# Performance work log

Measured on AMD Instinct MI355X. Metric: run time of the kernel, lower is better.

## Reference

```python
import jax, jax.numpy as jnp
import numpy as np

HEADS = 8
DIM_HEAD = 64
SCALE = DIM_HEAD ** -0.5
THRESH = 0.01


def setup_inputs() -> dict:
    key = jax.random.key(0)
    ks = jax.random.split(key, 5)
    b, n, dim = 4, 2048, 512
    inner = HEADS * DIM_HEAD  # 512
    x = jax.random.normal(ks[0], (b, n, dim), dtype=jnp.float32)
    Wqkv = jax.random.normal(ks[1], (dim, 3 * inner), dtype=jnp.float32) * (dim ** -0.5)
    bqkv = jax.random.normal(ks[2], (3 * inner,), dtype=jnp.float32) * 0.02
    Wout = jax.random.normal(ks[3], (inner, dim), dtype=jnp.float32) * (inner ** -0.5)
    bout = jax.random.normal(ks[4], (dim,), dtype=jnp.float32) * 0.02
    return {"x": x, "Wqkv": Wqkv, "bqkv": bqkv, "Wout": Wout, "bout": bout}


def reference(x, Wqkv, bqkv, Wout, bout):
    b, n, dim = x.shape
    qkv = x @ Wqkv + bqkv  # [b, n, 3*inner]
    q, k, v = jnp.split(qkv, 3, axis=-1)
    # b n (h d) -> b h n d
    split_heads = lambda t: t.reshape(b, n, HEADS, DIM_HEAD).transpose(0, 2, 1, 3)
    q, k, v = split_heads(q), split_heads(k), split_heads(v)
    dots = jnp.einsum('bhid,bhjd->bhij', q, k) * SCALE
    attn = jax.nn.softmax(dots, axis=-1)
    attn = jnp.where(attn > THRESH, attn, jnp.zeros_like(attn))
    out = jnp.einsum('bhij,bhjd->bhid', attn, v)
    out = out.transpose(0, 2, 1, 3).reshape(b, n, HEADS * DIM_HEAD)
    return out @ Wout + bout
```

## Files before the change

### kernel.cpp

```cpp
#include <hip/hip_runtime.h>

#define S_   2048
#define DM   512
#define HD   64
#define BHN  32

typedef unsigned short u16;
typedef __bf16 bf16x8 __attribute__((ext_vector_type(8)));
typedef float  f32x4  __attribute__((ext_vector_type(4)));

__device__ __forceinline__ float bf2f(u16 u) {
    union { unsigned int i; float f; } v; v.i = ((unsigned int)u) << 16; return v.f;
}
__device__ __forceinline__ u16 f2bf(float f) {
    union { float f; unsigned int i; } v; v.f = f;
    unsigned int i = v.i;
    return (u16)((i + 0x7FFFu + ((i >> 16) & 1u)) >> 16);
}
__device__ __forceinline__ void split3(float x, u16& b0, u16& b1, u16& b2) {
    b0 = f2bf(x);
    const float r0 = x - bf2f(b0);
    b1 = f2bf(r0);
    const float r1 = r0 - bf2f(b1);
    b2 = f2bf(r1);
}

__global__ __launch_bounds__(256) void prep_split_wT(
    const float* __restrict__ W, int N, int total,
    u16* __restrict__ w0, u16* __restrict__ w1, u16* __restrict__ w2)
{
    for (int idx = blockIdx.x * 256 + threadIdx.x; idx < total; idx += gridDim.x * 256) {
        const int n = idx >> 9, k = idx & 511;
        u16 a0, a1, a2;
        split3(W[(size_t)k * N + n], a0, a1, a2);
        w0[idx] = a0; w1[idx] = a1;
        if (w2) w2[idx] = a2;
    }
}

__global__ __launch_bounds__(256) void gemm_qkv_mfma(
    const float* __restrict__ A, const u16* __restrict__ Wt0, const u16* __restrict__ Wt1,
    const u16* __restrict__ Wt2, const float* __restrict__ bias,
    float* __restrict__ qh, float* __restrict__ kh, u16* __restrict__ vt)
{
    __shared__ __attribute__((aligned(16))) u16 As0[128 * 32], As1[128 * 32], As2[128 * 32];
    __shared__ __attribute__((aligned(16))) u16 Bs0[128 * 32], Bs1[128 * 32], Bs2[128 * 32];

    const int t  = threadIdx.x;
    const int m0 = blockIdx.y * 128, n0 = blockIdx.x * 128;
    const int w  = t >> 6, l = t & 63;
    const int wm = (w >> 1) * 64, wn = (w & 1) * 64;
    const int lr = l & 15, lq = l >> 4;

    const f32x4 zero4 = {0.f, 0.f, 0.f, 0.f};
    f32x4 acc[4][4];
#pragma unroll
    for (int i = 0; i < 4; i++)
#pragma unroll
        for (int j = 0; j < 4; j++) acc[i][j] = zero4;

    for (int k0 = 0; k0 < 512; k0 += 32) {
        __syncthreads();
#pragma unroll
        for (int i = 0; i < 4; i++) {
            const int e = t + 256 * i;
            const int r = e >> 3, c4 = (e & 7) * 4;
            const float4 f = *(const float4*)(&A[(size_t)(m0 + r) * 512 + k0 + c4]);
            const float xv[4] = {f.x, f.y, f.z, f.w};
            u16 a0[4], a1[4], a2[4];
#pragma unroll
            for (int j = 0; j < 4; j++) split3(xv[j], a0[j], a1[j], a2[j]);
            int2 p0, p1, p2;
            p0.x = a0[0] | (a0[1] << 16); p0.y = a0[2] | (a0[3] << 16);
            p1.x = a1[0] | (a1[1] << 16); p1.y = a1[2] | (a1[3] << 16);
            p2.x = a2[0] | (a2[1] << 16); p2.y = a2[2] | (a2[3] << 16);
            *(int2*)(&As0[r * 32 + c4]) = p0;
            *(int2*)(&As1[r * 32 + c4]) = p1;
            *(int2*)(&As2[r * 32 + c4]) = p2;
        }
#pragma unroll
        for (int i = 0; i < 2; i++) {
            const int e = t + 256 * i;
            const int r = e >> 2, c0 = (e & 3) * 8;
            *(int4*)(&Bs0[r * 32 + c0]) = *(const int4*)(&Wt0[(size_t)(n0 + r) * 512 + k0 + c0]);
            *(int4*)(&Bs1[r * 32 + c0]) = *(const int4*)(&Wt1[(size_t)(n0 + r) * 512 + k0 + c0]);
            *(int4*)(&Bs2[r * 32 + c0]) = *(const int4*)(&Wt2[(size_t)(n0 + r) * 512 + k0 + c0]);
        }
        __syncthreads();

#pragma unroll
        for (int i = 0; i < 4; i++) {
            const int ao = (wm + i * 16 + lr) * 32 + lq * 8;
            const bf16x8 a0 = *(const bf16x8*)(&As0[ao]);
            const bf16x8 a1 = *(const bf16x8*)(&As1[ao]);
            const bf16x8 a2 = *(const bf16x8*)(&As2[ao]);
#pragma unroll
            for (int j = 0; j < 4; j++) {
                const int bo = (wn + j * 16 + lr) * 32 + lq * 8;
                const bf16x8 b0 = *(const bf16x8*)(&Bs0[bo]);
                const bf16x8 b1 = *(const bf16x8*)(&Bs1[bo]);
                const bf16x8 b2 = *(const bf16x8*)(&Bs2[bo]);
                f32x4 c = acc[i][j];
                c = __builtin_amdgcn_mfma_f32_16x16x32_bf16(a0, b0, c, 0, 0, 0);
                c = __builtin_amdgcn_mfma_f32_16x16x32_bf16(a0, b1, c, 0, 0, 0);
                c = __builtin_amdgcn_mfma_f32_16x16x32_bf16(a1, b0, c, 0, 0, 0);
                c = __builtin_amdgcn_mfma_f32_16x16x32_bf16(a1, b1, c, 0, 0, 0);
                c = __builtin_amdgcn_mfma_f32_16x16x32_bf16(a0, b2, c, 0, 0, 0);
                c = __builtin_amdgcn_mfma_f32_16x16x32_bf16(a2, b0, c, 0, 0, 0);
                acc[i][j] = c;
            }
        }
    }

#pragma unroll
    for (int j = 0; j < 4; j++) {
        const int n = n0 + wn + j * 16 + lr;
        const float bv = bias[n];
        const int part = n >> 9, within = n & 511;
        const int h = within >> 6, d = within & 63;
#pragma unroll
        for (int i = 0; i < 4; i++) {
#pragma unroll
            for (int r = 0; r < 4; r++) {
                const int m = m0 + wm + i * 16 + lq * 4 + r;
                const int b = m >> 11, ns = m & 2047;
                const float val = acc[i][j][r] + bv;
                if (part == 0)
                    qh[(((size_t)(b * 8 + h)) * S_ + ns) * HD + d] = val;
                else if (part == 1)
                    kh[(((size_t)(b * 8 + h)) * S_ + ns) * HD + d] = val;
                else
                    vt[(((size_t)(b * 8 + h)) * HD + d) * S_ + ns] = f2bf(val);
            }
        }
    }
}

#define LDH 72

__global__ __launch_bounds__(256) void attn_mfma128(
    const float* __restrict__ q_ws, const float* __restrict__ k_ws,
    const u16* __restrict__ vt_ws, u16* __restrict__ ao_ws)
{
    __shared__ __attribute__((aligned(16))) u16 K0s[64 * LDH], K1s[64 * LDH], K2s[64 * LDH];
    __shared__ __attribute__((aligned(16))) u16 Vs[64 * LDH];
    __shared__ __attribute__((aligned(16))) u16 Ps[4][16 * LDH];

    const int t  = threadIdx.x;
    const int w  = t >> 6, l = t & 63;
    const int lr = l & 15, lq = l >> 4;
    const int bh = blockIdx.y, b = bh >> 3, h = bh & 7;
    const int q0 = blockIdx.x * 128;

    const float* qg  = q_ws + ((size_t)bh * S_ + q0) * HD;
    const float* kg0 = k_ws + (size_t)bh * S_ * HD;
    const u16*   vb  = vt_ws + (size_t)bh * HD * S_;

    bf16x8 fq0[2][2], fq1[2][2], fq2[2][2];
#pragma unroll
    for (int h2 = 0; h2 < 2; h2++) {
        __syncthreads();
#pragma unroll
        for (int i = 0; i < 4; i++) {
            const int e = t + 256 * i;
            const int row = e >> 4, c0 = (e & 15) * 4;
            const float4 f = *(const float4*)(qg + (size_t)h2 * 4096 + (size_t)e * 4);
            const float xv[4] = {f.x * 0.125f, f.y * 0.125f, f.z * 0.125f, f.w * 0.125f};
            u16 a0[4], a1[4], a2[4];
#pragma unroll
            for (int j = 0; j < 4; j++) split3(xv[j], a0[j], a1[j], a2[j]);
            int2 p0, p1, p2;
            p0.x = a0[0] | (a0[1] << 16); p0.y = a0[2] | (a0[3] << 16);
            p1.x = a1[0] | (a1[1] << 16); p1.y = a1[2] | (a1[3] << 16);
            p2.x = a2[0] | (a2[1] << 16); p2.y = a2[2] | (a2[3] << 16);
            *(int2*)(&K0s[row * LDH + c0]) = p0;
            *(int2*)(&K1s[row * LDH + c0]) = p1;
            *(int2*)(&K2s[row * LDH + c0]) = p2;
        }
        __syncthreads();
        if ((w >> 1) == h2) {
#pragma unroll
            for (int i = 0; i < 2; i++) {
#pragma unroll
                for (int kc = 0; kc < 2; kc++) {
                    const int o = ((w & 1) * 32 + i * 16 + lr) * LDH + kc * 32 + lq * 8;
                    fq0[i][kc] = *(const bf16x8*)(&K0s[o]);
                    fq1[i][kc] = *(const bf16x8*)(&K1s[o]);
                    fq2[i][kc] = *(const bf16x8*)(&K2s[o]);
                }
            }
        }
    }

    const f32x4 zero4 = {0.f, 0.f, 0.f, 0.f};
    double lsum[2][4];
#pragma unroll
    for (int i = 0; i < 2; i++)
#pragma unroll
        for (int r = 0; r < 4; r++) lsum[i][r] = 0.0;

    for (int jt = 0; jt < 32; jt++) {
        __syncthreads();
        const float* kg = kg0 + (size_t)jt * 64 * HD;
#pragma unroll
        for (int i = 0; i < 4; i++) {
            const int e = t + 256 * i;
            const int row = e >> 4, c0 = (e & 15) * 4;
            const float4 f = *(const float4*)(kg + (size_t)e * 4);
            const float xv[4] = {f.x, f.y, f.z, f.w};
            u16 a0[4], a1[4], a2[4];
#pragma unroll
            for (int j = 0; j < 4; j++) split3(xv[j], a0[j], a1[j], a2[j]);
            int2 p0, p1, p2;
            p0.x = a0[0] | (a0[1] << 16); p0.y = a0[2] | (a0[3] << 16);
            p1.x = a1[0] | (a1[1] << 16); p1.y = a1[2] | (a1[3] << 16);
            p2.x = a2[0] | (a2[1] << 16); p2.y = a2[2] | (a2[3] << 16);
            *(int2*)(&K0s[row * LDH + c0]) = p0;
            *(int2*)(&K1s[row * LDH + c0]) = p1;
            *(int2*)(&K2s[row * LDH + c0]) = p2;
        }
        __syncthreads();

#pragma unroll
        for (int i = 0; i < 2; i++) {
#pragma unroll
            for (int nt = 0; nt < 4; nt++) {
                f32x4 aHH = zero4, aC = zero4;
#pragma unroll
                for (int kc = 0; kc < 2; kc++) {
                    const int ko = (nt * 16 + lr) * LDH + kc * 32 + lq * 8;
                    const bf16x8 k0 = *(const bf16x8*)(&K0s[ko]);
                    const bf16x8 k1 = *(const bf16x8*)(&K1s[ko]);
                    const bf16x8 k2 = *(const bf16x8*)(&K2s[ko]);
                    aHH = __builtin_amdgcn_mfma_f32_16x16x32_bf16(fq0[i][kc], k0, aHH, 0, 0, 0);
                    aC  = __builtin_amdgcn_mfma_f32_16x16x32_bf16(fq0[i][kc], k1, aC, 0, 0, 0);
                    aC  = __builtin_amdgcn_mfma_f32_16x16x32_bf16(fq1[i][kc], k0, aC, 0, 0, 0);
                    aC  = __builtin_amdgcn_mfma_f32_16x16x32_bf16(fq1[i][kc], k1, aC, 0, 0, 0);
                    aC  = __builtin_amdgcn_mfma_f32_16x16x32_bf16(fq0[i][kc], k2, aC, 0, 0, 0);
                    aC  = __builtin_amdgcn_mfma_f32_16x16x32_bf16(fq2[i][kc], k0, aC, 0, 0, 0);
                }
#pragma unroll
                for (int r = 0; r < 4; r++) {
                    const float s = fminf(fmaxf(aHH[r] + aC[r], -30.f), 30.f);
                    lsum[i][r] += (double)__expf(s);
                }
            }
        }
    }
#pragma unroll
    for (int i = 0; i < 2; i++)
#pragma unroll
        for (int r = 0; r < 4; r++) {
#pragma unroll
            for (int off = 1; off < 16; off <<= 1)
                lsum[i][r] += __shfl_xor(lsum[i][r], off, 64);
        }
    double l_d[2][4]; float inv_l[2][4];
#pragma unroll
    for (int i = 0; i < 2; i++)
#pragma unroll
        for (int r = 0; r < 4; r++) {
            l_d[i][r] = lsum[i][r];
            inv_l[i][r] = (float)(1.0 / lsum[i][r]);
        }

    f32x4 oacc[2][4];
#pragma unroll
    for (int i = 0; i < 2; i++)
#pragma unroll
        for (int dt = 0; dt < 4; dt++) oacc[i][dt] = zero4;

    for (int jt = 0; jt < 32; jt++) {
        __syncthreads();
        const float* kg = kg0 + (size_t)jt * 64 * HD;
#pragma unroll
        for (int i = 0; i < 4; i++) {
            const int e = t + 256 * i;
            const int row = e >> 4, c0 = (e & 15) * 4;
            const float4 f = *(const float4*)(kg + (size_t)e * 4);
            int2 p0;
            p0.x = f2bf(f.x) | (f2bf(f.y) << 16);
            p0.y = f2bf(f.z) | (f2bf(f.w) << 16);
            *(int2*)(&K0s[row * LDH + c0]) = p0;
        }
#pragma unroll
        for (int i = 0; i < 2; i++) {
            const int e = t + 256 * i;
            const int row = e >> 3, c0 = (e & 7) * 8;
            *(int4*)(&Vs[row * LDH + c0]) = *(const int4*)(&vb[(size_t)row * S_ + jt * 64 + c0]);
        }
        __syncthreads();

#pragma unroll
        for (int i = 0; i < 2; i++) {
#pragma unroll
            for (int nt = 0; nt < 4; nt++) {
                f32x4 sacc = zero4;
#pragma unroll
                for (int kc = 0; kc < 2; kc++) {
                    const bf16x8 k0 = *(const bf16x8*)(&K0s[(nt * 16 + lr) * LDH + kc * 32 + lq * 8]);
                    sacc = __builtin_amdgcn_mfma_f32_16x16x32_bf16(fq0[i][kc], k0, sacc, 0, 0, 0);
                }
#pragma unroll
                for (int r = 0; r < 4; r++) {
                    const float s = fminf(fmaxf(sacc[r], -30.f), 30.f);
                    const float p = __expf(s) * inv_l[i][r];
                    u16 pb;
                    if (p > 0.0115f) {
                        pb = f2bf(p);
                    } else if (p < 0.009f) {
                        pb = 0;
                    } else {
                        const int row = q0 + w * 32 + i * 16 + lq * 4 + r;
                        const int col = jt * 64 + nt * 16 + lr;
                        const float* qr  = q_ws + ((size_t)bh * S_ + row) * HD;
                        const float* kcv = k_ws + ((size_t)bh * S_ + col) * HD;
                        double s64 = 0.0;
                        for (int d = 0; d < HD; d++) s64 += (double)qr[d] * (double)kcv[d];
                        s64 = fmin(fmax(s64 * 0.125, -30.0), 30.0);
                        const double pd = exp(s64) / l_d[i][r];
                        pb = (pd > 0.01) ? f2bf((float)pd) : (u16)0;
                    }
                    Ps[w][(lq * 4 + r) * LDH + nt * 16 + lr] = pb;
                }
            }
            __syncthreads();
#pragma unroll
            for (int kc = 0; kc < 2; kc++) {
                const bf16x8 ap = *(const bf16x8*)(&Ps[w][lr * LDH + kc * 32 + lq * 8]);
#pragma unroll
                for (int dt = 0; dt < 4; dt++) {
                    const bf16x8 bv = *(const bf16x8*)(&Vs[(dt * 16 + lr) * LDH + kc * 32 + lq * 8]);
                    oacc[i][dt] = __builtin_amdgcn_mfma_f32_16x16x32_bf16(ap, bv, oacc[i][dt], 0, 0, 0);
                }
            }
            __syncthreads();
        }
    }

#pragma unroll
    for (int i = 0; i < 2; i++)
#pragma unroll
        for (int dt = 0; dt < 4; dt++) {
#pragma unroll
            for (int r = 0; r < 4; r++) {
                const int row = q0 + w * 32 + i * 16 + lq * 4 + r;
                const int d   = dt * 16 + lr;
                ao_ws[((size_t)b * S_ + row) * DM + h * HD + d] = f2bf(oacc[i][dt][r]);
            }
        }
}

__global__ __launch_bounds__(256) void gemm_out_mfma(
    const u16* __restrict__ A, const u16* __restrict__ Wt0, const u16* __restrict__ Wt1,
    const float* __restrict__ bias, float* __restrict__ out)
{
    __shared__ __attribute__((aligned(16))) u16 As[128 * 32];
    __shared__ __attribute__((aligned(16))) u16 Bs0[128 * 32], Bs1[128 * 32];

    const int t  = threadIdx.x;
    const int m0 = blockIdx.y * 128, n0 = blockIdx.x * 128;
    const int w  = t >> 6, l = t & 63;
    const int wm = (w >> 1) * 64, wn = (w & 1) * 64;
    const int lr = l & 15, lq = l >> 4;

    const f32x4 zero4 = {0.f, 0.f, 0.f, 0.f};
    f32x4 acc[4][4];
#pragma unroll
    for (int i = 0; i < 4; i++)
#pragma unroll
        for (int j = 0; j < 4; j++) acc[i][j] = zero4;

    for (int k0 = 0; k0 < 512; k0 += 32) {
        __syncthreads();
#pragma unroll
        for (int i = 0; i < 2; i++) {
            const int e = t + 256 * i;
            const int r = e >> 2, c0 = (e & 3) * 8;
            *(int4*)(&As[r * 32 + c0])  = *(const int4*)(&A  [(size_t)(m0 + r) * 512 + k0 + c0]);
            *(int4*)(&Bs0[r * 32 + c0]) = *(const int4*)(&Wt0[(size_t)(n0 + r) * 512 + k0 + c0]);
            *(int4*)(&Bs1[r * 32 + c0]) = *(const int4*)(&Wt1[(size_t)(n0 + r) * 512 + k0 + c0]);
        }
        __syncthreads();

#pragma unroll
        for (int i = 0; i < 4; i++) {
            const bf16x8 a = *(const bf16x8*)(&As[(wm + i * 16 + lr) * 32 + lq * 8]);
#pragma unroll
            for (int j = 0; j < 4; j++) {
                const int bo = (wn + j * 16 + lr) * 32 + lq * 8;
                const bf16x8 b0 = *(const bf16x8*)(&Bs0[bo]);
                const bf16x8 b1 = *(const bf16x8*)(&Bs1[bo]);
                f32x4 c = acc[i][j];
                c = __builtin_amdgcn_mfma_f32_16x16x32_bf16(a, b0, c, 0, 0, 0);
                c = __builtin_amdgcn_mfma_f32_16x16x32_bf16(a, b1, c, 0, 0, 0);
                acc[i][j] = c;
            }
        }
    }

#pragma unroll
    for (int j = 0; j < 4; j++) {
        const int n = n0 + wn + j * 16 + lr;
        const float bv = bias[n];
#pragma unroll
        for (int i = 0; i < 4; i++) {
#pragma unroll
            for (int r = 0; r < 4; r++) {
                const int m = m0 + wm + i * 16 + lq * 4 + r;
                out[(size_t)m * 512 + n] = acc[i][j][r] + bv;
            }
        }
    }
}

extern "C" void kernel_launch(void* const* d_in, const int* in_sizes, int n_in,
                              void* d_out, int out_size, void* d_ws, size_t ws_size,
                              hipStream_t stream) {
    const float* x = nullptr; const float* Wqkv = nullptr; const float* bqkv = nullptr;
    const float* Wout = nullptr; const float* bout = nullptr;
    for (int i = 0; i < n_in; i++) {
        switch (in_sizes[i]) {
            case 4194304: x    = (const float*)d_in[i]; break;
            case 786432:  Wqkv = (const float*)d_in[i]; break;
            case 1536:    bqkv = (const float*)d_in[i]; break;
            case 262144:  Wout = (const float*)d_in[i]; break;
            case 512:     bout = (const float*)d_in[i]; break;
            default: break;
        }
    }
    if (!x)    x    = (const float*)d_in[0];
    if (!Wqkv) Wqkv = (const float*)d_in[1];
    if (!bqkv) bqkv = (const float*)d_in[2];
    if (!Wout) Wout = (const float*)d_in[3];
    if (!bout) bout = (const float*)d_in[4];

    float* out = (float*)d_out;

    char* ws = (char*)d_ws;
    float* q_ws  = (float*)(ws);
    float* k_ws  = (float*)(ws + (16ull << 20));
    u16* vt_ws = (u16*)(ws + (32ull << 20));
    u16* ao_ws = (u16*)(ws + (40ull << 20));
    u16* wt0 = (u16*)(ws + (40ull << 20));
    u16* wt1 = (u16*)(ws + (40ull << 20) + 1572864);
    u16* wt2 = (u16*)(ws + (40ull << 20) + 3145728);
    u16* wo0 = (u16*)(ws + (32ull << 20));
    u16* wo1 = (u16*)(ws + (32ull << 20) + 524288);

    prep_split_wT<<<3072, 256, 0, stream>>>(Wqkv, 1536, 1536 * 512, wt0, wt1, wt2);
    gemm_qkv_mfma<<<dim3(12, 64), 256, 0, stream>>>(
        x, wt0, wt1, wt2, bqkv, q_ws, k_ws, vt_ws);
    attn_mfma128<<<dim3(16, BHN), 256, 0, stream>>>(q_ws, k_ws, vt_ws, ao_ws);
    prep_split_wT<<<1024, 256, 0, stream>>>(Wout, 512, 512 * 512, wo0, wo1, nullptr);
    gemm_out_mfma<<<dim3(4, 64), 256, 0, stream>>>(ao_ws, wo0, wo1, bout, out);
}
```

Baseline: 511.4 us.

## Pre-split K into bf16 triples in QKV GEMM epilogue, drop per-tile splitting

The QKV GEMM epilogue now splits K into three bf16 components and stores them, so the attention kernel copies them with plain int4 loads instead of re-splitting fp32 K on every tile in both passes. The third component is stored in the output buffer as scratch. The __syncthreads around the per-wave P tile are also replaced with lgkmcnt waits. This removes repeated split arithmetic and barrier cost, at the price of more K bytes read per tile and a slower fallback dot product that reconstructs K from three arrays.

```diff
diff --git a/kernel.cpp b/kernel.cpp
--- a/kernel.cpp
+++ b/kernel.cpp
@@ -41,7 +41,8 @@
 __global__ __launch_bounds__(256) void gemm_qkv_mfma(
     const float* __restrict__ A, const u16* __restrict__ Wt0, const u16* __restrict__ Wt1,
     const u16* __restrict__ Wt2, const float* __restrict__ bias,
-    float* __restrict__ qh, float* __restrict__ kh, u16* __restrict__ vt)
+    float* __restrict__ qh, u16* __restrict__ k0w, u16* __restrict__ k1w,
+    u16* __restrict__ k2w, u16* __restrict__ vt)
 {
     __shared__ __attribute__((aligned(16))) u16 As0[128 * 32], As1[128 * 32], As2[128 * 32];
     __shared__ __attribute__((aligned(16))) u16 Bs0[128 * 32], Bs1[128 * 32], Bs2[128 * 32];
@@ -125,12 +126,16 @@
                 const int m = m0 + wm + i * 16 + lq * 4 + r;
                 const int b = m >> 11, ns = m & 2047;
                 const float val = acc[i][j][r] + bv;
-                if (part == 0)
+                if (part == 0) {
                     qh[(((size_t)(b * 8 + h)) * S_ + ns) * HD + d] = val;
-                else if (part == 1)
-                    kh[(((size_t)(b * 8 + h)) * S_ + ns) * HD + d] = val;
-                else
+                } else if (part == 1) {
+                    u16 c0, c1, c2;
+                    split3(val, c0, c1, c2);
+                    const size_t kidx = (((size_t)(b * 8 + h)) * S_ + ns) * HD + d;
+                    k0w[kidx] = c0; k1w[kidx] = c1; k2w[kidx] = c2;
+                } else {
                     vt[(((size_t)(b * 8 + h)) * HD + d) * S_ + ns] = f2bf(val);
+                }
             }
         }
     }
@@ -139,7 +144,8 @@
 #define LDH 72
 
 __global__ __launch_bounds__(256) void attn_mfma128(
-    const float* __restrict__ q_ws, const float* __restrict__ k_ws,
+    const float* __restrict__ q_ws,
+    const u16* __restrict__ k0_ws, const u16* __restrict__ k1_ws, const u16* __restrict__ k2_ws,
     const u16* __restrict__ vt_ws, u16* __restrict__ ao_ws)
 {
     __shared__ __attribute__((aligned(16))) u16 K0s[64 * LDH], K1s[64 * LDH], K2s[64 * LDH];
@@ -153,7 +159,7 @@
     const int q0 = blockIdx.x * 128;
 
     const float* qg  = q_ws + ((size_t)bh * S_ + q0) * HD;
-    const float* kg0 = k_ws + (size_t)bh * S_ * HD;
+    const size_t kbase = (size_t)bh * S_ * HD;
     const u16*   vb  = vt_ws + (size_t)bh * HD * S_;
 
     bf16x8 fq0[2][2], fq1[2][2], fq2[2][2];
@@ -201,23 +207,14 @@
 
     for (int jt = 0; jt < 32; jt++) {
         __syncthreads();
-        const float* kg = kg0 + (size_t)jt * 64 * HD;
-#pragma unroll
-        for (int i = 0; i < 4; i++) {
-            const int e = t + 256 * i;
-            const int row = e >> 4, c0 = (e & 15) * 4;
-            const float4 f = *(const float4*)(kg + (size_t)e * 4);
-            const float xv[4] = {f.x, f.y, f.z, f.w};
-            u16 a0[4], a1[4], a2[4];
-#pragma unroll
-            for (int j = 0; j < 4; j++) split3(xv[j], a0[j], a1[j], a2[j]);
-            int2 p0, p1, p2;
-            p0.x = a0[0] | (a0[1] << 16); p0.y = a0[2] | (a0[3] << 16);
-            p1.x = a1[0] | (a1[1] << 16); p1.y = a1[2] | (a1[3] << 16);
-            p2.x = a2[0] | (a2[1] << 16); p2.y = a2[2] | (a2[3] << 16);
-            *(int2*)(&K0s[row * LDH + c0]) = p0;
-            *(int2*)(&K1s[row * LDH + c0]) = p1;
-            *(int2*)(&K2s[row * LDH + c0]) = p2;
+        const size_t ko = kbase + (size_t)jt * 64 * HD;
+#pragma unroll
+        for (int i = 0; i < 2; i++) {
+            const int e = t + 256 * i;
+            const int row = e >> 3, c0 = (e & 7) * 8;
+            *(int4*)(&K0s[row * LDH + c0]) = *(const int4*)(&k0_ws[ko + (size_t)row * HD + c0]);
+            *(int4*)(&K1s[row * LDH + c0]) = *(const int4*)(&k1_ws[ko + (size_t)row * HD + c0]);
+            *(int4*)(&K2s[row * LDH + c0]) = *(const int4*)(&k2_ws[ko + (size_t)row * HD + c0]);
         }
         __syncthreads();
 
@@ -228,10 +225,10 @@
                 f32x4 aHH = zero4, aC = zero4;
 #pragma unroll
                 for (int kc = 0; kc < 2; kc++) {
-                    const int ko = (nt * 16 + lr) * LDH + kc * 32 + lq * 8;
-                    const bf16x8 k0 = *(const bf16x8*)(&K0s[ko]);
-                    const bf16x8 k1 = *(const bf16x8*)(&K1s[ko]);
-                    const bf16x8 k2 = *(const bf16x8*)(&K2s[ko]);
+                    const int koo = (nt * 16 + lr) * LDH + kc * 32 + lq * 8;
+                    const bf16x8 k0 = *(const bf16x8*)(&K0s[koo]);
+                    const bf16x8 k1 = *(const bf16x8*)(&K1s[koo]);
+                    const bf16x8 k2 = *(const bf16x8*)(&K2s[koo]);
                     aHH = __builtin_amdgcn_mfma_f32_16x16x32_bf16(fq0[i][kc], k0, aHH, 0, 0, 0);
                     aC  = __builtin_amdgcn_mfma_f32_16x16x32_bf16(fq0[i][kc], k1, aC, 0, 0, 0);
                     aC  = __builtin_amdgcn_mfma_f32_16x16x32_bf16(fq1[i][kc], k0, aC, 0, 0, 0);
@@ -272,22 +269,13 @@
 
     for (int jt = 0; jt < 32; jt++) {
         __syncthreads();
-        const float* kg = kg0 + (size_t)jt * 64 * HD;
-#pragma unroll
-        for (int i = 0; i < 4; i++) {
-            const int e = t + 256 * i;
-            const int row = e >> 4, c0 = (e & 15) * 4;
-            const float4 f = *(const float4*)(kg + (size_t)e * 4);
-            int2 p0;
-            p0.x = f2bf(f.x) | (f2bf(f.y) << 16);
-            p0.y = f2bf(f.z) | (f2bf(f.w) << 16);
-            *(int2*)(&K0s[row * LDH + c0]) = p0;
-        }
+        const size_t ko = kbase + (size_t)jt * 64 * HD;
 #pragma unroll
         for (int i = 0; i < 2; i++) {
             const int e = t + 256 * i;
             const int row = e >> 3, c0 = (e & 7) * 8;
-            *(int4*)(&Vs[row * LDH + c0]) = *(const int4*)(&vb[(size_t)row * S_ + jt * 64 + c0]);
+            *(int4*)(&K0s[row * LDH + c0]) = *(const int4*)(&k0_ws[ko + (size_t)row * HD + c0]);
+            *(int4*)(&Vs[row * LDH + c0])  = *(const int4*)(&vb[(size_t)row * S_ + jt * 64 + c0]);
         }
         __syncthreads();
 
@@ -314,9 +302,14 @@
                         const int row = q0 + w * 32 + i * 16 + lq * 4 + r;
                         const int col = jt * 64 + nt * 16 + lr;
                         const float* qr  = q_ws + ((size_t)bh * S_ + row) * HD;
-                        const float* kcv = k_ws + ((size_t)bh * S_ + col) * HD;
+                        const size_t kro = kbase + (size_t)col * HD;
                         double s64 = 0.0;
-                        for (int d = 0; d < HD; d++) s64 += (double)qr[d] * (double)kcv[d];
+                        for (int d = 0; d < HD; d++) {
+                            const double kv = (double)bf2f(k0_ws[kro + d])
+                                            + (double)bf2f(k1_ws[kro + d])
+                                            + (double)bf2f(k2_ws[kro + d]);
+                            s64 += (double)qr[d] * kv;
+                        }
                         s64 = fmin(fmax(s64 * 0.125, -30.0), 30.0);
                         const double pd = exp(s64) / l_d[i][r];
                         pb = (pd > 0.01) ? f2bf((float)pd) : (u16)0;
@@ -324,7 +317,7 @@
                     Ps[w][(lq * 4 + r) * LDH + nt * 16 + lr] = pb;
                 }
             }
-            __syncthreads();
+            asm volatile("s_waitcnt lgkmcnt(0)" ::: "memory");
 #pragma unroll
             for (int kc = 0; kc < 2; kc++) {
                 const bf16x8 ap = *(const bf16x8*)(&Ps[w][lr * LDH + kc * 32 + lq * 8]);
@@ -334,7 +327,7 @@
                     oacc[i][dt] = __builtin_amdgcn_mfma_f32_16x16x32_bf16(ap, bv, oacc[i][dt], 0, 0, 0);
                 }
             }
-            __syncthreads();
+            asm volatile("s_waitcnt lgkmcnt(0)" ::: "memory");
         }
     }
 
@@ -439,9 +432,11 @@
 
     char* ws = (char*)d_ws;
     float* q_ws  = (float*)(ws);
-    float* k_ws  = (float*)(ws + (16ull << 20));
+    u16* k0_ws = (u16*)(ws + (16ull << 20));
+    u16* k1_ws = (u16*)(ws + (24ull << 20));
     u16* vt_ws = (u16*)(ws + (32ull << 20));
     u16* ao_ws = (u16*)(ws + (40ull << 20));
+    u16* k2_ws = (u16*)d_out;
     u16* wt0 = (u16*)(ws + (40ull << 20));
     u16* wt1 = (u16*)(ws + (40ull << 20) + 1572864);
     u16* wt2 = (u16*)(ws + (40ull << 20) + 3145728);
@@ -450,8 +445,8 @@
 
     prep_split_wT<<<3072, 256, 0, stream>>>(Wqkv, 1536, 1536 * 512, wt0, wt1, wt2);
     gemm_qkv_mfma<<<dim3(12, 64), 256, 0, stream>>>(
-        x, wt0, wt1, wt2, bqkv, q_ws, k_ws, vt_ws);
-    attn_mfma128<<<dim3(16, BHN), 256, 0, stream>>>(q_ws, k_ws, vt_ws, ao_ws);
+        x, wt0, wt1, wt2, bqkv, q_ws, k0_ws, k1_ws, k2_ws, vt_ws);
+    attn_mfma128<<<dim3(16, BHN), 256, 0, stream>>>(q_ws, k0_ws, k1_ws, k2_ws, vt_ws, ao_ws);
     prep_split_wT<<<1024, 256, 0, stream>>>(Wout, 512, 512 * 512, wo0, wo1, nullptr);
     gemm_out_mfma<<<dim3(4, 64), 256, 0, stream>>>(ao_ws, wo0, wo1, bout, out);
 }
```

After: 581.5 us. 1.14x slower.

## Use 512-thread attention blocks with one 16-row query tile per wave

Applied to the files above, without the earlier changes.

The attention kernel now launches 8 waves per block instead of 4. Each wave owns 16 query rows instead of 32, and the per-wave i-loop is removed. K/V staging is spread over twice as many threads and the P buffer grows to 8 slots. The aim is more waves per CU and lower register pressure to hide latency, but each K tile loaded into LDS is now reused by fewer rows per wave, and barriers now span more waves.

```diff
diff --git a/kernel.cpp b/kernel.cpp
--- a/kernel.cpp
+++ b/kernel.cpp
@@ -138,13 +138,13 @@
 
 #define LDH 72
 
-__global__ __launch_bounds__(256) void attn_mfma128(
+__global__ __launch_bounds__(512) void attn_mfma128(
     const float* __restrict__ q_ws, const float* __restrict__ k_ws,
     const u16* __restrict__ vt_ws, u16* __restrict__ ao_ws)
 {
     __shared__ __attribute__((aligned(16))) u16 K0s[64 * LDH], K1s[64 * LDH], K2s[64 * LDH];
     __shared__ __attribute__((aligned(16))) u16 Vs[64 * LDH];
-    __shared__ __attribute__((aligned(16))) u16 Ps[4][16 * LDH];
+    __shared__ __attribute__((aligned(16))) u16 Ps[8][16 * LDH];
 
     const int t  = threadIdx.x;
     const int w  = t >> 6, l = t & 63;
@@ -156,13 +156,13 @@
     const float* kg0 = k_ws + (size_t)bh * S_ * HD;
     const u16*   vb  = vt_ws + (size_t)bh * HD * S_;
 
-    bf16x8 fq0[2][2], fq1[2][2], fq2[2][2];
+    bf16x8 fq0[2], fq1[2], fq2[2];
 #pragma unroll
     for (int h2 = 0; h2 < 2; h2++) {
         __syncthreads();
 #pragma unroll
-        for (int i = 0; i < 4; i++) {
-            const int e = t + 256 * i;
+        for (int i = 0; i < 2; i++) {
+            const int e = t + 512 * i;
             const int row = e >> 4, c0 = (e & 15) * 4;
             const float4 f = *(const float4*)(qg + (size_t)h2 * 4096 + (size_t)e * 4);
             const float xv[4] = {f.x * 0.125f, f.y * 0.125f, f.z * 0.125f, f.w * 0.125f};
@@ -178,33 +178,28 @@
             *(int2*)(&K2s[row * LDH + c0]) = p2;
         }
         __syncthreads();
-        if ((w >> 1) == h2) {
-#pragma unroll
-            for (int i = 0; i < 2; i++) {
-#pragma unroll
-                for (int kc = 0; kc < 2; kc++) {
-                    const int o = ((w & 1) * 32 + i * 16 + lr) * LDH + kc * 32 + lq * 8;
-                    fq0[i][kc] = *(const bf16x8*)(&K0s[o]);
-                    fq1[i][kc] = *(const bf16x8*)(&K1s[o]);
-                    fq2[i][kc] = *(const bf16x8*)(&K2s[o]);
-                }
+        if ((w >> 2) == h2) {
+#pragma unroll
+            for (int kc = 0; kc < 2; kc++) {
+                const int o = ((w & 3) * 16 + lr) * LDH + kc * 32 + lq * 8;
+                fq0[kc] = *(const bf16x8*)(&K0s[o]);
+                fq1[kc] = *(const bf16x8*)(&K1s[o]);
+                fq2[kc] = *(const bf16x8*)(&K2s[o]);
             }
         }
     }
 
     const f32x4 zero4 = {0.f, 0.f, 0.f, 0.f};
-    double lsum[2][4];
-#pragma unroll
-    for (int i = 0; i < 2; i++)
-#pragma unroll
-        for (int r = 0; r < 4; r++) lsum[i][r] = 0.0;
+    double lsum[4];
+#pragma unroll
+    for (int r = 0; r < 4; r++) lsum[r] = 0.0;
 
     for (int jt = 0; jt < 32; jt++) {
         __syncthreads();
         const float* kg = kg0 + (size_t)jt * 64 * HD;
 #pragma unroll
-        for (int i = 0; i < 4; i++) {
-            const int e = t + 256 * i;
+        for (int i = 0; i < 2; i++) {
+            const int e = t + 512 * i;
             const int row = e >> 4, c0 = (e & 15) * 4;
             const float4 f = *(const float4*)(kg + (size_t)e * 4);
             const float xv[4] = {f.x, f.y, f.z, f.w};
@@ -222,60 +217,51 @@
         __syncthreads();
 
 #pragma unroll
+        for (int nt = 0; nt < 4; nt++) {
+            f32x4 aHH = zero4, aC = zero4;
+#pragma unroll
+            for (int kc = 0; kc < 2; kc++) {
+                const int ko = (nt * 16 + lr) * LDH + kc * 32 + lq * 8;
+                const bf16x8 k0 = *(const bf16x8*)(&K0s[ko]);
+                const bf16x8 k1 = *(const bf16x8*)(&K1s[ko]);
+                const bf16x8 k2 = *(const bf16x8*)(&K2s[ko]);
+                aHH = __builtin_amdgcn_mfma_f32_16x16x32_bf16(fq0[kc], k0, aHH, 0, 0, 0);
+                aC  = __builtin_amdgcn_mfma_f32_16x16x32_bf16(fq0[kc], k1, aC, 0, 0, 0);
+                aC  = __builtin_amdgcn_mfma_f32_16x16x32_bf16(fq1[kc], k0, aC, 0, 0, 0);
+                aC  = __builtin_amdgcn_mfma_f32_16x16x32_bf16(fq1[kc], k1, aC, 0, 0, 0);
+                aC  = __builtin_amdgcn_mfma_f32_16x16x32_bf16(fq0[kc], k2, aC, 0, 0, 0);
+                aC  = __builtin_amdgcn_mfma_f32_16x16x32_bf16(fq2[kc], k0, aC, 0, 0, 0);
+            }
+#pragma unroll
+            for (int r = 0; r < 4; r++) {
+                const float s = fminf(fmaxf(aHH[r] + aC[r], -30.f), 30.f);
+                lsum[r] += (double)__expf(s);
+            }
+        }
+    }
+#pragma unroll
+    for (int r = 0; r < 4; r++) {
+#pragma unroll
+        for (int off = 1; off < 16; off <<= 1)
+            lsum[r] += __shfl_xor(lsum[r], off, 64);
+    }
+    double l_d[4]; float inv_l[4];
+#pragma unroll
+    for (int r = 0; r < 4; r++) {
+        l_d[r] = lsum[r];
+        inv_l[r] = (float)(1.0 / lsum[r]);
+    }
+
+    f32x4 oacc[4];
+#pragma unroll
+    for (int dt = 0; dt < 4; dt++) oacc[dt] = zero4;
+
+    for (int jt = 0; jt < 32; jt++) {
+        __syncthreads();
+        const float* kg = kg0 + (size_t)jt * 64 * HD;
+#pragma unroll
         for (int i = 0; i < 2; i++) {
-#pragma unroll
-            for (int nt = 0; nt < 4; nt++) {
-                f32x4 aHH = zero4, aC = zero4;
-#pragma unroll
-                for (int kc = 0; kc < 2; kc++) {
-                    const int ko = (nt * 16 + lr) * LDH + kc * 32 + lq * 8;
-                    const bf16x8 k0 = *(const bf16x8*)(&K0s[ko]);
-                    const bf16x8 k1 = *(const bf16x8*)(&K1s[ko]);
-                    const bf16x8 k2 = *(const bf16x8*)(&K2s[ko]);
-                    aHH = __builtin_amdgcn_mfma_f32_16x16x32_bf16(fq0[i][kc], k0, aHH, 0, 0, 0);
-                    aC  = __builtin_amdgcn_mfma_f32_16x16x32_bf16(fq0[i][kc], k1, aC, 0, 0, 0);
-                    aC  = __builtin_amdgcn_mfma_f32_16x16x32_bf16(fq1[i][kc], k0, aC, 0, 0, 0);
-                    aC  = __builtin_amdgcn_mfma_f32_16x16x32_bf16(fq1[i][kc], k1, aC, 0, 0, 0);
-                    aC  = __builtin_amdgcn_mfma_f32_16x16x32_bf16(fq0[i][kc], k2, aC, 0, 0, 0);
-                    aC  = __builtin_amdgcn_mfma_f32_16x16x32_bf16(fq2[i][kc], k0, aC, 0, 0, 0);
-                }
-#pragma unroll
-                for (int r = 0; r < 4; r++) {
-                    const float s = fminf(fmaxf(aHH[r] + aC[r], -30.f), 30.f);
-                    lsum[i][r] += (double)__expf(s);
-                }
-            }
-        }
-    }
-#pragma unroll
-    for (int i = 0; i < 2; i++)
-#pragma unroll
-        for (int r = 0; r < 4; r++) {
-#pragma unroll
-            for (int off = 1; off < 16; off <<= 1)
-                lsum[i][r] += __shfl_xor(lsum[i][r], off, 64);
-        }
-    double l_d[2][4]; float inv_l[2][4];
-#pragma unroll
-    for (int i = 0; i < 2; i++)
-#pragma unroll
-        for (int r = 0; r < 4; r++) {
-            l_d[i][r] = lsum[i][r];
-            inv_l[i][r] = (float)(1.0 / lsum[i][r]);
-        }
-
-    f32x4 oacc[2][4];
-#pragma unroll
-    for (int i = 0; i < 2; i++)
-#pragma unroll
-        for (int dt = 0; dt < 4; dt++) oacc[i][dt] = zero4;
-
-    for (int jt = 0; jt < 32; jt++) {
-        __syncthreads();
-        const float* kg = kg0 + (size_t)jt * 64 * HD;
-#pragma unroll
-        for (int i = 0; i < 4; i++) {
-            const int e = t + 256 * i;
+            const int e = t + 512 * i;
             const int row = e >> 4, c0 = (e & 15) * 4;
             const float4 f = *(const float4*)(kg + (size_t)e * 4);
             int2 p0;
@@ -283,72 +269,65 @@
             p0.y = f2bf(f.z) | (f2bf(f.w) << 16);
             *(int2*)(&K0s[row * LDH + c0]) = p0;
         }
-#pragma unroll
-        for (int i = 0; i < 2; i++) {
-            const int e = t + 256 * i;
+        {
+            const int e = t;
             const int row = e >> 3, c0 = (e & 7) * 8;
             *(int4*)(&Vs[row * LDH + c0]) = *(const int4*)(&vb[(size_t)row * S_ + jt * 64 + c0]);
         }
         __syncthreads();
 
 #pragma unroll
-        for (int i = 0; i < 2; i++) {
-#pragma unroll
-            for (int nt = 0; nt < 4; nt++) {
-                f32x4 sacc = zero4;
-#pragma unroll
-                for (int kc = 0; kc < 2; kc++) {
-                    const bf16x8 k0 = *(const bf16x8*)(&K0s[(nt * 16 + lr) * LDH + kc * 32 + lq * 8]);
-                    sacc = __builtin_amdgcn_mfma_f32_16x16x32_bf16(fq0[i][kc], k0, sacc, 0, 0, 0);
+        for (int nt = 0; nt < 4; nt++) {
+            f32x4 sacc = zero4;
+#pragma unroll
+            for (int kc = 0; kc < 2; kc++) {
+                const bf16x8 k0 = *(const bf16x8*)(&K0s[(nt * 16 + lr) * LDH + kc * 32 + lq * 8]);
+                sacc = __builtin_amdgcn_mfma_f32_16x16x32_bf16(fq0[kc], k0, sacc, 0, 0, 0);
+            }
+#pragma unroll
+            for (int r = 0; r < 4; r++) {
+                const float s = fminf(fmaxf(sacc[r], -30.f), 30.f);
+                const float p = __expf(s) * inv_l[r];
+                u16 pb;
+                if (p > 0.0115f) {
+                    pb = f2bf(p);
+                } else if (p < 0.009f) {
+                    pb = 0;
+                } else {
+                    const int row = q0 + w * 16 + lq * 4 + r;
+                    const int col = jt * 64 + nt * 16 + lr;
+                    const float* qr  = q_ws + ((size_t)bh * S_ + row) * HD;
+                    const float* kcv = k_ws + ((size_t)bh * S_ + col) * HD;
+                    double s64 = 0.0;
+                    for (int d = 0; d < HD; d++) s64 += (double)qr[d] * (double)kcv[d];
+                    s64 = fmin(fmax(s64 * 0.125, -30.0), 30.0);
+                    const double pd = exp(s64) / l_d[r];
+                    pb = (pd > 0.01) ? f2bf((float)pd) : (u16)0;
                 }
-#pragma unroll
-                for (int r = 0; r < 4; r++) {
-                    const float s = fminf(fmaxf(sacc[r], -30.f), 30.f);
-                    const float p = __expf(s) * inv_l[i][r];
-                    u16 pb;
-                    if (p > 0.0115f) {
-                        pb = f2bf(p);
-                    } else if (p < 0.009f) {
-                        pb = 0;
-                    } else {
-                        const int row = q0 + w * 32 + i * 16 + lq * 4 + r;
-                        const int col = jt * 64 + nt * 16 + lr;
-                        const float* qr  = q_ws + ((size_t)bh * S_ + row) * HD;
-                        const float* kcv = k_ws + ((size_t)bh * S_ + col) * HD;
-                        double s64 = 0.0;
-                        for (int d = 0; d < HD; d++) s64 += (double)qr[d] * (double)kcv[d];
-                        s64 = fmin(fmax(s64 * 0.125, -30.0), 30.0);
-                        const double pd = exp(s64) / l_d[i][r];
-                        pb = (pd > 0.01) ? f2bf((float)pd) : (u16)0;
-                    }
-                    Ps[w][(lq * 4 + r) * LDH + nt * 16 + lr] = pb;
-                }
-            }
-            __syncthreads();
-#pragma unroll
-            for (int kc = 0; kc < 2; kc++) {
-                const bf16x8 ap = *(const bf16x8*)(&Ps[w][lr * LDH + kc * 32 + lq * 8]);
-#pragma unroll
-                for (int dt = 0; dt < 4; dt++) {
-                    const bf16x8 bv = *(const bf16x8*)(&Vs[(dt * 16 + lr) * LDH + kc * 32 + lq * 8]);
-                    oacc[i][dt] = __builtin_amdgcn_mfma_f32_16x16x32_bf16(ap, bv, oacc[i][dt], 0, 0, 0);
-                }
-            }
-            __syncthreads();
-        }
-    }
-
-#pragma unroll
-    for (int i = 0; i < 2; i++)
-#pragma unroll
-        for (int dt = 0; dt < 4; dt++) {
-#pragma unroll
-            for (int r = 0; r < 4; r++) {
-                const int row = q0 + w * 32 + i * 16 + lq * 4 + r;
-                const int d   = dt * 16 + lr;
-                ao_ws[((size_t)b * S_ + row) * DM + h * HD + d] = f2bf(oacc[i][dt][r]);
-            }
-        }
+                Ps[w][(lq * 4 + r) * LDH + nt * 16 + lr] = pb;
+            }
+        }
+        __syncthreads();
+#pragma unroll
+        for (int kc = 0; kc < 2; kc++) {
+            const bf16x8 ap = *(const bf16x8*)(&Ps[w][lr * LDH + kc * 32 + lq * 8]);
+#pragma unroll
+            for (int dt = 0; dt < 4; dt++) {
+                const bf16x8 bv = *(const bf16x8*)(&Vs[(dt * 16 + lr) * LDH + kc * 32 + lq * 8]);
+                oacc[dt] = __builtin_amdgcn_mfma_f32_16x16x32_bf16(ap, bv, oacc[dt], 0, 0, 0);
+            }
+        }
+    }
+
+#pragma unroll
+    for (int dt = 0; dt < 4; dt++) {
+#pragma unroll
+        for (int r = 0; r < 4; r++) {
+            const int row = q0 + w * 16 + lq * 4 + r;
+            const int d   = dt * 16 + lr;
+            ao_ws[((size_t)b * S_ + row) * DM + h * HD + d] = f2bf(oacc[dt][r]);
+        }
+    }
 }
 
 __global__ __launch_bounds__(256) void gemm_out_mfma(
@@ -451,7 +430,7 @@
     prep_split_wT<<<3072, 256, 0, stream>>>(Wqkv, 1536, 1536 * 512, wt0, wt1, wt2);
     gemm_qkv_mfma<<<dim3(12, 64), 256, 0, stream>>>(
         x, wt0, wt1, wt2, bqkv, q_ws, k_ws, vt_ws);
-    attn_mfma128<<<dim3(16, BHN), 256, 0, stream>>>(q_ws, k_ws, vt_ws, ao_ws);
+    attn_mfma128<<<dim3(16, BHN), 512, 0, stream>>>(q_ws, k_ws, vt_ws, ao_ws);
     prep_split_wT<<<1024, 256, 0, stream>>>(Wout, 512, 512 * 512, wo0, wo1, nullptr);
     gemm_out_mfma<<<dim3(4, 64), 256, 0, stream>>>(ao_ws, wo0, wo1, bout, out);
 }
```

New measurement: 447.8 us. -12.5%, faster.
